# Performance work log

Hardware: AMD Instinct MI355X
Metric: run time of the kernel (lower is better)

Reference implementation:

```python
import jax, jax.numpy as jnp
import numpy as np
from functools import partial

B, CI, HI, WI = 128, 3, 128, 128
G = 12
HG, WG = 16, 16
HIDLIN = 512
CH1, CH2, CH3 = 32, 64, 128
HID = (HI // 8) * (WI // 8) * CH3  # after maxpool(4) then maxpool(2)
SIGMA_BOOST = 2.0
EPS = 1e-7


def conv3x3(x, w, b):
    # x: NCHW, w: OIHW, padding=1 (same)
    y = jax.lax.conv_general_dilated(x, w, (1, 1), [(1, 1), (1, 1)],
                                     dimension_numbers=('NCHW', 'OIHW', 'NCHW'))
    return y + b[None, :, None, None]


def maxpool(x, k):
    return jax.lax.reduce_window(x, -jnp.inf, jax.lax.max,
                                 (1, 1, k, k), (1, 1, k, k), 'VALID')


def setup_inputs() -> dict:
    key = jax.random.key(0)
    ks = jax.random.split(key, 12)

    def w(k, shape, fan_in):
        return (jax.random.normal(k, shape, jnp.float32) / np.float32(np.sqrt(fan_in)))

    return {
        'image': jax.random.normal(ks[0], (B, CI, HI, WI), jnp.float32),
        'noise': jax.random.normal(ks[1], (B, G, 2), jnp.float32),
        'w1': w(ks[2], (CH1, CI, 3, 3), CI * 9), 'b1': jnp.zeros((CH1,), jnp.float32),
        'w2': w(ks[3], (CH1, CH1, 3, 3), CH1 * 9), 'b2': jnp.zeros((CH1,), jnp.float32),
        'w3': w(ks[4], (CH2, CH1, 3, 3), CH1 * 9), 'b3': jnp.zeros((CH2,), jnp.float32),
        'w4': w(ks[5], (CH2, CH2, 3, 3), CH2 * 9), 'b4': jnp.zeros((CH2,), jnp.float32),
        'w5': w(ks[6], (CH3, CH2, 3, 3), CH2 * 9), 'b5': jnp.zeros((CH3,), jnp.float32),
        'w6': w(ks[7], (CH3, CH3, 3, 3), CH3 * 9), 'b6': jnp.zeros((CH3,), jnp.float32),
        'wl1': w(ks[8], (HID, HIDLIN), HID), 'bl1': jnp.zeros((HIDLIN,), jnp.float32),
        'wl2': w(ks[9], (HIDLIN, HIDLIN), HIDLIN), 'bl2': jnp.zeros((HIDLIN,), jnp.float32),
        'wl3': w(ks[10], (HIDLIN, G * 3), HIDLIN), 'bl3': jnp.zeros((G * 3,), jnp.float32),
    }


def preprocess(image, w1, b1, w2, b2, w3, b3, w4, b4, w5, b5, w6, b6,
               wl1, bl1, wl2, bl2, wl3, bl3):
    r = jax.nn.relu
    x = r(conv3x3(image, w1, b1))
    x = r(conv3x3(x, w2, b2))
    x = maxpool(x, 4)
    x = r(conv3x3(x, w3, b3))
    x = r(conv3x3(x, w4, b4))
    x = maxpool(x, 2)
    x = r(conv3x3(x, w5, b5))
    x = r(conv3x3(x, w6, b6))
    x = x.reshape(x.shape[0], -1)          # (B, HID)
    x = x @ wl1 + bl1                       # Linear(HID, 512)
    x = r(x)
    x = x @ wl2 + bl2                       # Linear(512, 512)
    x = r(x)                                # extra ReLU before head
    x = x @ wl3 + bl3                       # Linear(512, G*3)
    return x.reshape(x.shape[0], G, 3)


def reference(image, noise, w1, b1, w2, b2, w3, b3, w4, b4, w5, b5, w6, b6,
              wl1, bl1, wl2, bl2, wl3, bl3):
    prep = preprocess(image, w1, b1, w2, b2, w3, b3, w4, b4, w5, b5, w6, b6,
                      wl1, bl1, wl2, bl2, wl3, bl3)     # (B, G, 3)
    means = prep[:, :, :2]                               # (B, G, 2)
    # transform_sigmas: softplus(s + SIGMA_BOOST) scaled by image dims
    sizes = jnp.array([HI, WI], jnp.float32)
    sigmas = jax.nn.softplus(prep[:, :, 2] + SIGMA_BOOST)[:, :, None] * sizes + EPS
    # reparameterized Normal sample (torch .sample() draw made explicit)
    sample = means + sigmas * noise                      # (B, G, 2)
    # transform_means (sigmoid): scale to [0, size-1], then round to int
    rng = jnp.array([HI - HG, WI - WG], jnp.float32) - 1.0
    pts = jnp.round(jax.nn.sigmoid(sample) * rng).astype(jnp.int32)  # (B, G, 2)

    def extract(img, hw):
        return jax.lax.dynamic_slice(img, (0, hw[0], hw[1]), (CI, HG, WG))

    # vectorized batched glimpse gather: (B, G, CI, HG, WG)
    result = jax.vmap(lambda img, p: jax.vmap(partial(extract, img))(p))(image, pts)
    return result, means, sigmas, sample
```

## Files before the change

### kernel.cpp

```cpp
#include <hip/hip_runtime.h>
#include <math.h>

typedef _Float16 __attribute__((ext_vector_type(8))) half8_t;
typedef _Float16 __attribute__((ext_vector_type(4))) half4_t;
typedef _Float16 __attribute__((ext_vector_type(2))) half2_t;
typedef float    __attribute__((ext_vector_type(4))) float4_t;

#define POSP 336

__device__ __forceinline__ int c1idx(int slot, int pos) {
    return ((slot * POSP + pos) * 8) ^ (((pos >> 3) & 7) << 3);
}

__global__ __launch_bounds__(256, 5)
void k_conv12(const float* __restrict__ img, const float* __restrict__ b1,
              const _Float16* __restrict__ B1h, const _Float16* __restrict__ B1l,
              const _Float16* __restrict__ B2h, const _Float16* __restrict__ B2l,
              const float* __restrict__ b2,
              _Float16* __restrict__ P1h, _Float16* __restrict__ P1l)
{
    __shared__ float simg[3 * 20 * 25];
    __shared__ __align__(16) _Float16 C1h[4 * POSP * 8];

    const int t  = threadIdx.x;
    const int bt = blockIdx.x;
    const int b  = blockIdx.y;
    const int ty = bt >> 3, tx = bt & 7;
    const int oy = ty * 16, ox = tx * 16;

    for (int i = t; i < 1500; i += 256) {
        const int ci = i / 500, r = i - ci * 500;
        const int yy = r / 25, xx = r - yy * 25;
        const int gy = oy - 2 + yy, gx = ox - 2 + xx;
        float v = 0.f;
        if ((unsigned)gy < 128u && (unsigned)gx < 128u)
            v = img[((b * 3 + ci) * 128 + gy) * 128 + gx];
        simg[i] = v;
    }
    __syncthreads();

    #pragma unroll
    for (int hf = 0; hf < 2; ++hf) {
        const int pos = hf * 256 + t;
        if (pos < POSP) {
            const bool val = pos < 324;
            int sb = 0;
            if (val) {
                const int py = pos / 18, px = pos - py * 18;
                sb = py * 25 + px;
            }
            #pragma unroll
            for (int s = 0; s < 4; ++s) {
                half8_t vh = {0,0,0,0,0,0,0,0};
                if (val) {
                    #pragma unroll
                    for (int j = 0; j < 8; ++j) {
                        const int k = s * 8 + j;
                        if (k < 27) {
                            const int ci = k / 9, tap = k - ci * 9;
                            const int dy = tap / 3, dx = tap - dy * 3;
                            vh[j] = (_Float16)simg[sb + (ci * 20 + dy) * 25 + dx];
                        }
                    }
                }
                *(half8_t*)(&C1h[c1idx(s, pos)]) = vh;
            }
        }
    }
    __syncthreads();

    const int wv   = __builtin_amdgcn_readfirstlane(t >> 6);
    const int lane = t & 63;
    const int fr   = lane >> 4;
    const int ml   = lane & 15;

    half8_t wAh[2], wAl[2];
    #pragma unroll
    for (int mt = 0; mt < 2; ++mt) {
        wAh[mt] = *(const half8_t*)(B1h + (mt * 64 + lane) * 8);
        wAl[mt] = *(const half8_t*)(B1l + (mt * 64 + lane) * 8);
    }
    float4_t acc1[6][2];
    #pragma unroll
    for (int q = 0; q < 6; ++q)
        #pragma unroll
        for (int mt = 0; mt < 2; ++mt)
            acc1[q][mt] = (float4_t){0.f, 0.f, 0.f, 0.f};

    #pragma unroll
    for (int q = 0; q < 6; ++q) {
        const int nt = wv + q * 4;
        if (nt < 21) {
            const int ri = c1idx(fr, nt * 16 + ml);
            const half8_t dh = *(const half8_t*)(&C1h[ri]);
            #pragma unroll
            for (int mt = 0; mt < 2; ++mt) {
                acc1[q][mt] = __builtin_amdgcn_mfma_f32_16x16x32_f16(wAh[mt], dh, acc1[q][mt], 0, 0, 0);
                acc1[q][mt] = __builtin_amdgcn_mfma_f32_16x16x32_f16(wAl[mt], dh, acc1[q][mt], 0, 0, 0);
            }
        }
    }
    __syncthreads();

    const float4_t bA = *(const float4_t*)(b1 + fr * 4);
    const float4_t bB = *(const float4_t*)(b1 + 16 + fr * 4);
    #pragma unroll
    for (int q = 0; q < 6; ++q) {
        const int nt = wv + q * 4;
        if (nt < 21) {
            const int pos = nt * 16 + ml;
            if (pos < 324) {
                const int py = pos / 18, px = pos - py * 18;
                const int gy = oy + py - 1, gx = ox + px - 1;
                const bool ok = (unsigned)gy < 128u && (unsigned)gx < 128u;
                #pragma unroll
                for (int mt = 0; mt < 2; ++mt) {
                    const int slot = mt * 2 + (fr >> 1);
                    const int wi = c1idx(slot, pos) + (fr & 1) * 4;
                    const float4_t bb = mt ? bB : bA;
                    half4_t oh;
                    #pragma unroll
                    for (int r = 0; r < 4; ++r) {
                        const float v = ok ? fmaxf(acc1[q][mt][r] + bb[r], 0.f) : 0.f;
                        oh[r] = (_Float16)v;
                    }
                    *(half4_t*)(&C1h[wi]) = oh;
                }
            }
        }
    }
    __syncthreads();

    float4_t acc[4][2];
    #pragma unroll
    for (int i = 0; i < 4; ++i)
        #pragma unroll
        for (int nt = 0; nt < 2; ++nt)
            acc[i][nt] = (float4_t){0.f, 0.f, 0.f, 0.f};

    #pragma unroll 1
    for (int tap = 0; tap < 9; ++tap) {
        const int dy = tap / 3, dx = tap - dy * 3;
        half8_t bh[2], bl[2];
        #pragma unroll
        for (int nt = 0; nt < 2; ++nt) {
            const int bo = ((tap * 2 + nt) * 64 + lane) * 8;
            bh[nt] = *(const half8_t*)(B2h + bo);
            bl[nt] = *(const half8_t*)(B2l + bo);
        }
        half8_t ah[4];
        #pragma unroll
        for (int i = 0; i < 4; ++i) {
            const int pos = (wv * 4 + i + dy) * 18 + ml + dx;
            ah[i] = *(const half8_t*)(&C1h[c1idx(fr, pos)]);
        }
        #pragma unroll
        for (int nt = 0; nt < 2; ++nt)
            #pragma unroll
            for (int i = 0; i < 4; ++i)
                acc[i][nt] = __builtin_amdgcn_mfma_f32_16x16x32_f16(ah[i], bh[nt], acc[i][nt], 0, 0, 0);
        #pragma unroll
        for (int nt = 0; nt < 2; ++nt)
            #pragma unroll
            for (int i = 0; i < 4; ++i)
                acc[i][nt] = __builtin_amdgcn_mfma_f32_16x16x32_f16(ah[i], bl[nt], acc[i][nt], 0, 0, 0);
    }

    const int py = ty * 4 + wv;
    const int px = tx * 4 + fr;
    #pragma unroll
    for (int nt = 0; nt < 2; ++nt) {
        float m = -1e30f;
        #pragma unroll
        for (int i = 0; i < 4; ++i)
            #pragma unroll
            for (int r = 0; r < 4; ++r)
                m = fmaxf(m, acc[i][nt][r]);
        const int oc = nt * 16 + ml;
        const float v = fmaxf(m + b2[oc], 0.f);
        const _Float16 h = (_Float16)v;
        const int base = ((b * 32 + py) * 32 + px) * 32 + oc;
        P1h[base] = h;
        P1l[base] = (_Float16)(v - (float)h);
    }
}

__global__ void k_wrepackm(const float* __restrict__ w1, const float* __restrict__ w2,
                           const float* __restrict__ w3, const float* __restrict__ w4,
                           const float* __restrict__ w5, const float* __restrict__ w6,
                           _Float16* __restrict__ Bh, _Float16* __restrict__ Bl,
                           _Float16* __restrict__ B1h, _Float16* __restrict__ B1l)
{
    int idx = blockIdx.x * 256 + threadIdx.x;
    if (idx >= 285696) {
        const int i = idx - 285696;
        if (i >= 1024) return;
        const int ntg = i >> 9, rr = i & 511;
        const int lane = rr >> 3, j = rr & 7;
        const int k = (lane >> 4) * 8 + j;
        const int n = ntg * 16 + (lane & 15);
        const float v = (k < 27) ? w1[n * 27 + k] : 0.f;
        const _Float16 h = (_Float16)v;
        B1h[i] = h;
        B1l[i] = (_Float16)(v - (float)h);
        return;
    }
    const float* w; int CIN, COUT, off;
    if (idx < 9216)        { w = w2; CIN = 32;  COUT = 32;  off = 0; }
    else if (idx < 27648)  { idx -= 9216;   w = w3; CIN = 32;  COUT = 64;  off = 9216; }
    else if (idx < 64512)  { idx -= 27648;  w = w4; CIN = 64;  COUT = 64;  off = 27648; }
    else if (idx < 138240) { idx -= 64512;  w = w5; CIN = 64;  COUT = 128; off = 64512; }
    else                   { idx -= 138240; w = w6; CIN = 128; COUT = 128; off = 138240; }
    const int NT  = COUT / 16;
    const int c   = idx / (NT * 512);
    const int r   = idx - c * NT * 512;
    const int ntg = r >> 9;
    const int rr  = r & 511;
    const int lane = rr >> 3, j = rr & 7;
    const int k   = c * 32 + (lane >> 4) * 8 + j;
    const int tap = k / CIN, ci = k - tap * CIN;
    const int oc  = ntg * 16 + (lane & 15);
    const float v = w[(oc * CIN + ci) * 9 + tap];
    const _Float16 h = (_Float16)v;
    Bh[off + idx] = h;
    Bl[off + idx] = (_Float16)(v - (float)h);
}

template<int CIN, int COUT, int HW, bool OUTF32, int BK>
__global__ __launch_bounds__(256, 2)
void k_mgemm(const _Float16* __restrict__ inh, const _Float16* __restrict__ inl,
             const _Float16* __restrict__ Bh, const _Float16* __restrict__ Bl,
             const float* __restrict__ bias,
             _Float16* __restrict__ outh, _Float16* __restrict__ outl,
             float* __restrict__ outf)
{
    constexpr int NCH = CIN * 9 / BK;
    constexpr int SUB = BK / 32;
    constexpr int NT  = COUT / 16;
    constexpr int LOG = (HW == 32) ? 5 : 4;
    constexpr int PS  = BK + ((BK == 64) ? 4 : 8);
    constexpr int NJ  = BK / 16;
    constexpr int GPR = BK / 8;
    __shared__ _Float16 Ash[128 * PS];
    __shared__ _Float16 Asl[128 * PS];

    const int t    = threadIdx.x;
    const int wv   = t >> 6;
    const int lane = t & 63;
    const int m0   = blockIdx.x * 128;
    const int nb   = blockIdx.y;

    int sm[NJ], sg[NJ], sb[NJ], sy[NJ], sx[NJ];
    #pragma unroll
    for (int j = 0; j < NJ; ++j) {
        const int q = t + 256 * j;
        sm[j] = q / GPR;
        sg[j] = q - sm[j] * GPR;
        const int m  = m0 + sm[j];
        const int yx = m & (HW * HW - 1);
        sb[j] = m >> (2 * LOG);
        sy[j] = yx >> LOG;
        sx[j] = yx & (HW - 1);
    }

    const int mt0 = wv * 2;
    const int fr  = lane >> 4;
    const int ml  = lane & 15;

    float4_t acc[2][4];
    #pragma unroll
    for (int mt = 0; mt < 2; ++mt)
        #pragma unroll
        for (int tn = 0; tn < 4; ++tn)
            acc[mt][tn] = (float4_t){0.f, 0.f, 0.f, 0.f};

    #pragma unroll 1
    for (int ch = 0; ch < NCH; ++ch) {
        const int kb  = ch * BK;
        const int tap = kb / CIN;
        const int c0  = kb - tap * CIN;
        const int dy  = tap / 3 - 1, dx = tap - (tap / 3) * 3 - 1;

        if (ch) __syncthreads();
        #pragma unroll
        for (int j = 0; j < NJ; ++j) {
            const int iy = sy[j] + dy, ix = sx[j] + dx;
            half8_t vh = {0, 0, 0, 0, 0, 0, 0, 0};
            half8_t vl = {0, 0, 0, 0, 0, 0, 0, 0};
            if ((unsigned)iy < (unsigned)HW && (unsigned)ix < (unsigned)HW) {
                const int o = ((sb[j] * HW + iy) * HW + ix) * CIN + c0 + sg[j] * 8;
                vh = *(const half8_t*)(inh + o);
                vl = *(const half8_t*)(inl + o);
            }
            *(half8_t*)(&Ash[sm[j] * PS + sg[j] * 8]) = vh;
            *(half8_t*)(&Asl[sm[j] * PS + sg[j] * 8]) = vl;
        }
        __syncthreads();

        #pragma unroll
        for (int ss = 0; ss < SUB; ++ss) {
            half8_t ah[2], al[2];
            #pragma unroll
            for (int mt = 0; mt < 2; ++mt) {
                const int mr = (mt0 + mt) * 16 + ml;
                ah[mt] = *(const half8_t*)(&Ash[mr * PS + ss * 32 + fr * 8]);
                al[mt] = *(const half8_t*)(&Asl[mr * PS + ss * 32 + fr * 8]);
            }
            half8_t bh[4], bl[4];
            #pragma unroll
            for (int tn = 0; tn < 4; ++tn) {
                const int bo = (((ch * SUB + ss) * NT + nb * 4 + tn) * 64 + lane) * 8;
                bh[tn] = *(const half8_t*)(Bh + bo);
                bl[tn] = *(const half8_t*)(Bl + bo);
            }
            #pragma unroll
            for (int tn = 0; tn < 4; ++tn)
                #pragma unroll
                for (int mt = 0; mt < 2; ++mt)
                    acc[mt][tn] = __builtin_amdgcn_mfma_f32_16x16x32_f16(ah[mt], bh[tn], acc[mt][tn], 0, 0, 0);
            #pragma unroll
            for (int tn = 0; tn < 4; ++tn)
                #pragma unroll
                for (int mt = 0; mt < 2; ++mt)
                    acc[mt][tn] = __builtin_amdgcn_mfma_f32_16x16x32_f16(al[mt], bh[tn], acc[mt][tn], 0, 0, 0);
            #pragma unroll
            for (int tn = 0; tn < 4; ++tn)
                #pragma unroll
                for (int mt = 0; mt < 2; ++mt)
                    acc[mt][tn] = __builtin_amdgcn_mfma_f32_16x16x32_f16(ah[mt], bl[tn], acc[mt][tn], 0, 0, 0);
        }
    }

    #pragma unroll
    for (int mt = 0; mt < 2; ++mt)
        #pragma unroll
        for (int tn = 0; tn < 4; ++tn) {
            const int oc = nb * 64 + tn * 16 + ml;
            const float bv = bias[oc];
            #pragma unroll
            for (int r = 0; r < 4; ++r) {
                const int m = m0 + (mt0 + mt) * 16 + fr * 4 + r;
                const float v = fmaxf(acc[mt][tn][r] + bv, 0.f);
                if (OUTF32) {
                    outf[m * COUT + oc] = v;
                } else {
                    const _Float16 h = (_Float16)v;
                    outh[m * COUT + oc] = h;
                    outl[m * COUT + oc] = (_Float16)(v - (float)h);
                }
            }
        }
}

__global__ __launch_bounds__(256)
void k_pool2h(const _Float16* __restrict__ inh, const _Float16* __restrict__ inl,
              _Float16* __restrict__ outh, _Float16* __restrict__ outl)
{
    const int g = blockIdx.x * 256 + threadIdx.x;
    const int c4 = g & 15, xo = (g >> 4) & 15, yo = (g >> 8) & 15, b = g >> 12;
    const int base = ((b * 32 + yo * 2) * 32 + xo * 2) * 64 + c4 * 4;
    const int offs[4] = {0, 64, 2048, 2112};
    float mx[4] = {-1e30f, -1e30f, -1e30f, -1e30f};
    #pragma unroll
    for (int cnd = 0; cnd < 4; ++cnd) {
        const half4_t h = *(const half4_t*)(inh + base + offs[cnd]);
        const half4_t l = *(const half4_t*)(inl + base + offs[cnd]);
        #pragma unroll
        for (int e = 0; e < 4; ++e)
            mx[e] = fmaxf(mx[e], (float)h[e] + (float)l[e]);
    }
    half4_t oh, ol;
    #pragma unroll
    for (int e = 0; e < 4; ++e) {
        const _Float16 h = (_Float16)mx[e];
        oh[e] = h;
        ol[e] = (_Float16)(mx[e] - (float)h);
    }
    const int ob = ((b * 16 + yo) * 16 + xo) * 64 + c4 * 4;
    *(half4_t*)(outh + ob) = oh;
    *(half4_t*)(outl + ob) = ol;
}

template<int LDA, int KCHUNK, int TN, bool PERM>
__global__ __launch_bounds__(256, 2)
void k_fc_partial(const float* __restrict__ A, const float* __restrict__ Bw,
                  float* __restrict__ part)
{
    constexpr int BN = 16 * TN;
    constexpr int SA = 140;
    constexpr int SB = (BN == 128) ? 140 : 68;
    __shared__ __align__(16) float As[32 * SA];
    __shared__ __align__(16) float Bs[32 * SB];
    const int t  = threadIdx.x;
    const int tm = t >> 4, tn = t & 15;
    const int n0 = blockIdx.x * BN;
    const int k0 = blockIdx.y * KCHUNK;

    float acc[8][TN];
    #pragma unroll
    for (int r = 0; r < 8; ++r)
        #pragma unroll
        for (int c = 0; c < TN; ++c) acc[r][c] = 0.f;

    #pragma unroll 1
    for (int ks = 0; ks < KCHUNK / 32; ++ks) {
        if (ks) __syncthreads();
        const int kb = k0 + ks * 32;
        for (int i = t; i < 4096; i += 256) {
            const int m = i >> 5, kk = i & 31;
            As[kk * SA + m + ((m >> 5) << 2)] = A[m * LDA + kb + kk];
        }
        for (int i = t; i < 32 * BN; i += 256) {
            const int kk = i / BN, n = i - kk * BN;
            const int krow = kb + kk;
            const int kref = PERM ? ((krow & 127) * 256 + (krow >> 7)) : krow;
            Bs[kk * SB + n + ((n >> 5) << 2)] = Bw[kref * 512 + n0 + n];
        }
        __syncthreads();
        #pragma unroll 2
        for (int kk = 0; kk < 32; ++kk) {
            const float* ap = &As[kk * SA + tm * 8 + ((tm >> 2) << 2)];
            const float* bp = &Bs[kk * SB + tn * TN + (((tn * TN) >> 5) << 2)];
            float a[8], bb[TN];
            #pragma unroll
            for (int q = 0; q < 8; q += 4) {
                const float4 v = *(const float4*)(ap + q);
                a[q] = v.x; a[q + 1] = v.y; a[q + 2] = v.z; a[q + 3] = v.w;
            }
            #pragma unroll
            for (int q = 0; q < TN; q += 4) {
                const float4 v = *(const float4*)(bp + q);
                bb[q] = v.x; bb[q + 1] = v.y; bb[q + 2] = v.z; bb[q + 3] = v.w;
            }
            #pragma unroll
            for (int r = 0; r < 8; ++r)
                #pragma unroll
                for (int c = 0; c < TN; ++c)
                    acc[r][c] = fmaf(a[r], bb[c], acc[r][c]);
        }
    }

    const long pb = (long)blockIdx.y * 65536;
    #pragma unroll
    for (int r = 0; r < 8; ++r)
        #pragma unroll
        for (int c = 0; c < TN; ++c)
            part[pb + (tm * 8 + r) * 512 + n0 + tn * TN + c] = acc[r][c];
}

template<int NS>
__global__ __launch_bounds__(256)
void k_fc_reduce(const float* __restrict__ part, const float* __restrict__ bias,
                 float* __restrict__ H)
{
    const int f = (blockIdx.x * 256 + threadIdx.x) * 4;
    const int m = f >> 9, n = f & 511;
    float s0 = 0.f, s1 = 0.f, s2 = 0.f, s3 = 0.f;
    #pragma unroll 4
    for (int q = 0; q < NS; ++q) {
        const float* p = &part[(q * 128 + m) * 512 + n];
        s0 += p[0]; s1 += p[1]; s2 += p[2]; s3 += p[3];
    }
    H[f]     = fmaxf(s0 + bias[n],     0.f);
    H[f + 1] = fmaxf(s1 + bias[n + 1], 0.f);
    H[f + 2] = fmaxf(s2 + bias[n + 2], 0.f);
    H[f + 3] = fmaxf(s3 + bias[n + 3], 0.f);
}

__device__ __forceinline__ float softplusf(float x) {
    return (x > 20.f) ? x : log1pf(expf(x));
}
__device__ __forceinline__ float sigmoidf_(float x) {
    return 1.f / (1.f + expf(-x));
}

__global__ __launch_bounds__(256)
void k_final(const float* __restrict__ H2, const float* __restrict__ wl3,
             const float* __restrict__ bl3, const float* __restrict__ noise,
             const float* __restrict__ img, float* __restrict__ outp)
{
    __shared__ float h2[512];
    __shared__ float red[144];
    __shared__ float prep[36];
    __shared__ int ptsh[12], ptsw[12];
    const int b = blockIdx.x, t = threadIdx.x;

    h2[t]       = H2[b * 512 + t];
    h2[t + 256] = H2[b * 512 + 256 + t];
    __syncthreads();

    if (t < 144) {
        const int n = t >> 2, q = t & 3;
        float s = 0.f;
        for (int k = q * 128; k < q * 128 + 128; ++k)
            s = fmaf(h2[k], wl3[k * 36 + n], s);
        red[t] = s;
    }
    __syncthreads();
    if (t < 36)
        prep[t] = red[t * 4] + red[t * 4 + 1] + red[t * 4 + 2] + red[t * 4 + 3] + bl3[t];
    __syncthreads();

    if (t < 12) {
        const float m0 = prep[t * 3], m1 = prep[t * 3 + 1], sv = prep[t * 3 + 2];
        const float sig = softplusf(sv + 2.0f) * 128.f + 1e-7f;
        const float n0 = noise[(b * 12 + t) * 2], n1 = noise[(b * 12 + t) * 2 + 1];
        const float sa0 = m0 + sig * n0;
        const float sa1 = m1 + sig * n1;
        int p0 = (int)rintf(sigmoidf_(sa0) * 111.f);
        int p1 = (int)rintf(sigmoidf_(sa1) * 111.f);
        p0 = min(max(p0, 0), 111);
        p1 = min(max(p1, 0), 111);
        const int RM = 1179648;
        outp[RM        + (b * 12 + t) * 2 + 0] = m0;
        outp[RM        + (b * 12 + t) * 2 + 1] = m1;
        outp[RM + 3072 + (b * 12 + t) * 2 + 0] = sig;
        outp[RM + 3072 + (b * 12 + t) * 2 + 1] = sig;
        outp[RM + 6144 + (b * 12 + t) * 2 + 0] = sa0;
        outp[RM + 6144 + (b * 12 + t) * 2 + 1] = sa1;
        ptsh[t] = p0;
        ptsw[t] = p1;
    }
    __syncthreads();

    for (int i = t; i < 9216; i += 256) {
        const int g  = i / 768, r = i - g * 768;
        const int c  = r >> 8, r2 = r & 255;
        const int y  = r2 >> 4, x = r2 & 15;
        outp[b * 9216 + i] = img[((b * 3 + c) * 128 + ptsh[g] + y) * 128 + (ptsw[g] + x)];
    }
}

extern "C" void kernel_launch(void* const* d_in, const int* in_sizes, int n_in,
                              void* d_out, int out_size, void* d_ws, size_t ws_size,
                              hipStream_t stream)
{
    const float* img  = (const float*)d_in[0];
    const float* nois = (const float*)d_in[1];
    const float* w1 = (const float*)d_in[2];  const float* b1 = (const float*)d_in[3];
    const float* w2 = (const float*)d_in[4];  const float* b2 = (const float*)d_in[5];
    const float* w3 = (const float*)d_in[6];  const float* b3 = (const float*)d_in[7];
    const float* w4 = (const float*)d_in[8];  const float* b4 = (const float*)d_in[9];
    const float* w5 = (const float*)d_in[10]; const float* b5 = (const float*)d_in[11];
    const float* w6 = (const float*)d_in[12]; const float* b6 = (const float*)d_in[13];
    const float* wl1 = (const float*)d_in[14]; const float* bl1 = (const float*)d_in[15];
    const float* wl2 = (const float*)d_in[16]; const float* bl2 = (const float*)d_in[17];
    const float* wl3 = (const float*)d_in[18]; const float* bl3 = (const float*)d_in[19];
    float* out = (float*)d_out;
    float* ws  = (float*)d_ws;

    _Float16* P1h = (_Float16*)(ws);
    _Float16* P1l = (_Float16*)(ws + 2097152);
    _Float16* A3h = (_Float16*)(ws + 4194304);
    _Float16* A3l = (_Float16*)(ws + 8388608);
    _Float16* A4h = (_Float16*)(ws + 12582912);
    _Float16* A4l = (_Float16*)(ws + 16777216);
    _Float16* P2h = (_Float16*)(ws);
    _Float16* P2l = (_Float16*)(ws + 1048576);
    _Float16* A5h = (_Float16*)(ws + 4194304);
    _Float16* A5l = (_Float16*)(ws + 6291456);
    float* A6  = ws + 8388608;
    float* FP1 = ws + 12582912;
    float* H1  = ws + 16777216;
    float* FP2 = ws + 16842752;
    float* H2  = ws + 17891328;
    _Float16* B1h = (_Float16*)(ws + 17956864);
    _Float16* B1l = (_Float16*)(ws + 17957376);
    _Float16* Bh = (_Float16*)(ws + 20971520);
    _Float16* Bl = (_Float16*)(ws + 21114368);

    hipLaunchKernelGGL(k_wrepackm, dim3(1120), dim3(256), 0, stream,
                       w1, w2, w3, w4, w5, w6, Bh, Bl, B1h, B1l);

    hipLaunchKernelGGL(k_conv12, dim3(64, 128), dim3(256), 0, stream,
                       img, b1, B1h, B1l, Bh + 0, Bl + 0, b2, P1h, P1l);
    hipLaunchKernelGGL((k_mgemm<32, 64, 32, false, 32>), dim3(1024, 1), dim3(256), 0, stream,
                       P1h, P1l, Bh + 9216, Bl + 9216, b3, A3h, A3l, nullptr);
    hipLaunchKernelGGL((k_mgemm<64, 64, 32, false, 64>), dim3(1024, 1), dim3(256), 0, stream,
                       A3h, A3l, Bh + 27648, Bl + 27648, b4, A4h, A4l, nullptr);
    hipLaunchKernelGGL(k_pool2h, dim3(2048), dim3(256), 0, stream, A4h, A4l, P2h, P2l);
    hipLaunchKernelGGL((k_mgemm<64, 128, 16, false, 64>), dim3(256, 2), dim3(256), 0, stream,
                       P2h, P2l, Bh + 64512, Bl + 64512, b5, A5h, A5l, nullptr);
    hipLaunchKernelGGL((k_mgemm<128, 128, 16, true, 64>), dim3(256, 2), dim3(256), 0, stream,
                       A5h, A5l, Bh + 138240, Bl + 138240, b6, nullptr, nullptr, A6);
    hipLaunchKernelGGL((k_fc_partial<32768, 512, 4, true>), dim3(8, 64), dim3(256), 0, stream,
                       A6, wl1, FP1);
    hipLaunchKernelGGL(k_fc_reduce<64>, dim3(64), dim3(256), 0, stream, FP1, bl1, H1);
    hipLaunchKernelGGL((k_fc_partial<512, 32, 4, false>), dim3(8, 16), dim3(256), 0, stream,
                       H1, wl2, FP2);
    hipLaunchKernelGGL(k_fc_reduce<16>, dim3(64), dim3(256), 0, stream, FP2, bl2, H2);
    hipLaunchKernelGGL(k_final, dim3(128), dim3(256), 0, stream,
                       H2, wl3, bl3, nois, img, out);
}
```

Baseline: 550.1 us.

## Compute first FC layer with split-fp16 MFMA instead of fp32 partial kernel

The conv6 output is now stored as fp16 hi/lo pairs instead of fp32. A new split-K kernel computes the large first linear layer with 3-term fp16 MFMA (hi*hi, lo*hi, hi*lo), splitting the fp32 weights into hi/lo on the fly in shared memory. This replaces the scalar fp32 partial-sum kernel for the 32768x512 GEMM and is meant to cut its compute time. The cost is that the weights are still read as fp32 and converted every call, plus some precision loss from the 3-term split.

Result: faster. 470.8 us (-14.4%).

```diff
diff --git a/kernel.cpp b/kernel.cpp
--- a/kernel.cpp
+++ b/kernel.cpp
@@ -352,6 +352,112 @@
         }
 }
 
+__global__ __launch_bounds__(256, 2)
+void k_fc1m(const _Float16* __restrict__ A6h, const _Float16* __restrict__ A6l,
+            const float* __restrict__ wl1, float* __restrict__ part)
+{
+    __shared__ __align__(16) _Float16 Ah[128 * 68];
+    __shared__ __align__(16) _Float16 Al[128 * 68];
+    __shared__ __align__(16) _Float16 Wh[64 * 68];
+    __shared__ __align__(16) _Float16 Wl[64 * 68];
+
+    const int t    = threadIdx.x;
+    const int wv   = t >> 6;
+    const int lane = t & 63;
+    const int fr   = lane >> 4;
+    const int ml   = lane & 15;
+    const int n0   = blockIdx.x * 64;
+    const int kc   = blockIdx.y;
+
+    float4_t acc[2][4];
+    #pragma unroll
+    for (int mt = 0; mt < 2; ++mt)
+        #pragma unroll
+        for (int tn = 0; tn < 4; ++tn)
+            acc[mt][tn] = (float4_t){0.f, 0.f, 0.f, 0.f};
+
+    #pragma unroll 1
+    for (int it = 0; it < 8; ++it) {
+        const int kb = kc * 512 + it * 64;
+        const int yx = kb >> 7;
+        const int c0 = kb & 127;
+
+        if (it) __syncthreads();
+        #pragma unroll
+        for (int q = 0; q < 4; ++q) {
+            const int lin = q * 256 + t;
+            const int bb = lin >> 3, g = lin & 7;
+            const int src = (bb * 256 + yx) * 128 + c0 + g * 8;
+            *(half8_t*)(&Ah[bb * 68 + g * 8]) = *(const half8_t*)(A6h + src);
+            *(half8_t*)(&Al[bb * 68 + g * 8]) = *(const half8_t*)(A6l + src);
+        }
+        {
+            const int kk = t >> 2;
+            const float* wrow = wl1 + ((c0 + kk) * 256 + yx) * 512 + n0;
+            #pragma unroll
+            for (int q = 0; q < 4; ++q) {
+                const int nq = (t & 3) + q * 4;
+                const float4 v = *(const float4*)(wrow + nq * 4);
+                #pragma unroll
+                for (int e = 0; e < 4; ++e) {
+                    const int n = nq * 4 + e;
+                    const float w = (&v.x)[e];
+                    const _Float16 h = (_Float16)w;
+                    Wh[n * 68 + kk] = h;
+                    Wl[n * 68 + kk] = (_Float16)(w - (float)h);
+                }
+            }
+        }
+        __syncthreads();
+
+        #pragma unroll
+        for (int ss = 0; ss < 2; ++ss) {
+            half8_t ah[2], al[2];
+            #pragma unroll
+            for (int mt = 0; mt < 2; ++mt) {
+                const int bb = (wv * 2 + mt) * 16 + ml;
+                ah[mt] = *(const half8_t*)(&Ah[bb * 68 + ss * 32 + fr * 8]);
+                al[mt] = *(const half8_t*)(&Al[bb * 68 + ss * 32 + fr * 8]);
+            }
+            half8_t bh[4], bl[4];
+            #pragma unroll
+            for (int tn = 0; tn < 4; ++tn) {
+                const int nn = tn * 16 + ml;
+                bh[tn] = *(const half8_t*)(&Wh[nn * 68 + ss * 32 + fr * 8]);
+                bl[tn] = *(const half8_t*)(&Wl[nn * 68 + ss * 32 + fr * 8]);
+            }
+            #pragma unroll
+            for (int tn = 0; tn < 4; ++tn)
+                #pragma unroll
+                for (int mt = 0; mt < 2; ++mt)
+                    acc[mt][tn] = __builtin_amdgcn_mfma_f32_16x16x32_f16(ah[mt], bh[tn], acc[mt][tn], 0, 0, 0);
+            #pragma unroll
+            for (int tn = 0; tn < 4; ++tn)
+                #pragma unroll
+                for (int mt = 0; mt < 2; ++mt)
+                    acc[mt][tn] = __builtin_amdgcn_mfma_f32_16x16x32_f16(al[mt], bh[tn], acc[mt][tn], 0, 0, 0);
+            #pragma unroll
+            for (int tn = 0; tn < 4; ++tn)
+                #pragma unroll
+                for (int mt = 0; mt < 2; ++mt)
+                    acc[mt][tn] = __builtin_amdgcn_mfma_f32_16x16x32_f16(ah[mt], bl[tn], acc[mt][tn], 0, 0, 0);
+        }
+    }
+
+    const long pb = (long)kc * 65536;
+    #pragma unroll
+    for (int mt = 0; mt < 2; ++mt)
+        #pragma unroll
+        for (int tn = 0; tn < 4; ++tn) {
+            const int nn = n0 + tn * 16 + ml;
+            #pragma unroll
+            for (int r = 0; r < 4; ++r) {
+                const int m = (wv * 2 + mt) * 16 + fr * 4 + r;
+                part[pb + m * 512 + nn] = acc[mt][tn][r];
+            }
+        }
+}
+
 __global__ __launch_bounds__(256)
 void k_pool2h(const _Float16* __restrict__ inh, const _Float16* __restrict__ inl,
               _Float16* __restrict__ outh, _Float16* __restrict__ outl)
@@ -559,7 +665,8 @@
     _Float16* P2l = (_Float16*)(ws + 1048576);
     _Float16* A5h = (_Float16*)(ws + 4194304);
     _Float16* A5l = (_Float16*)(ws + 6291456);
-    float* A6  = ws + 8388608;
+    _Float16* A6h = (_Float16*)(ws + 8388608);
+    _Float16* A6l = (_Float16*)(ws + 10485760);
     float* FP1 = ws + 12582912;
     float* H1  = ws + 16777216;
     float* FP2 = ws + 16842752;
@@ -581,10 +688,10 @@
     hipLaunchKernelGGL(k_pool2h, dim3(2048), dim3(256), 0, stream, A4h, A4l, P2h, P2l);
     hipLaunchKernelGGL((k_mgemm<64, 128, 16, false, 64>), dim3(256, 2), dim3(256), 0, stream,
                        P2h, P2l, Bh + 64512, Bl + 64512, b5, A5h, A5l, nullptr);
-    hipLaunchKernelGGL((k_mgemm<128, 128, 16, true, 64>), dim3(256, 2), dim3(256), 0, stream,
-                       A5h, A5l, Bh + 138240, Bl + 138240, b6, nullptr, nullptr, A6);
-    hipLaunchKernelGGL((k_fc_partial<32768, 512, 4, true>), dim3(8, 64), dim3(256), 0, stream,
-                       A6, wl1, FP1);
+    hipLaunchKernelGGL((k_mgemm<128, 128, 16, false, 64>), dim3(256, 2), dim3(256), 0, stream,
+                       A5h, A5l, Bh + 138240, Bl + 138240, b6, A6h, A6l, nullptr);
+    hipLaunchKernelGGL(k_fc1m, dim3(8, 64), dim3(256), 0, stream,
+                       A6h, A6l, wl1, FP1);
     hipLaunchKernelGGL(k_fc_reduce<64>, dim3(64), dim3(256), 0, stream, FP1, bl1, H1);
     hipLaunchKernelGGL((k_fc_partial<512, 32, 4, false>), dim3(8, 16), dim3(256), 0, stream,
                        H1, wl2, FP2);
```
